# Performance work log

Hardware: AMD Instinct MI355X
Metric: run time of the kernel (lower is better)

The kernel has to match this reference:

```python
import jax, jax.numpy as jnp
import numpy as np

B, T, P, D, H = 32, 64, 196, 768, 12
HD = D // H   # MHA head dim = 64
F = D // H    # GAT per-head out features = 64


def _grid_adj(num_patches):
    g = int(np.sqrt(num_patches))
    a = np.zeros((num_patches, num_patches), np.int32)
    for i in range(num_patches):
        a[i, i] = 1
        r, c = divmod(i, g)
        for dr in (-1, 0, 1):
            for dc in (-1, 0, 1):
                if dr == 0 and dc == 0:
                    continue
                nr, nc = r + dr, c + dc
                if 0 <= nr < g and 0 <= nc < g:
                    a[i, nr * g + nc] = 1
    return a


def setup_inputs():
    key = jax.random.key(0)
    ks = jax.random.split(key, 32)
    s = 0.02
    ta = jax.random.randint(ks[2], (B, T, T), 0, 2).astype(jnp.int32)
    ta = jnp.maximum(jnp.maximum(ta, ta.transpose(0, 2, 1)), jnp.eye(T, dtype=jnp.int32))
    return {
        'text_features': jax.random.normal(ks[0], (B, T, D), jnp.float32),
        'image_features': jax.random.normal(ks[1], (B, P, D), jnp.float32),
        'clip_text': jax.random.normal(ks[3], (B, 512), jnp.float32),
        'clip_image': jax.random.normal(ks[4], (B, 512), jnp.float32),
        'logit_scale': jnp.float32(4.6052),  # ln(100), CLIP default
        'wq': jax.random.normal(ks[5], (D, D), jnp.float32) * s,
        'bq': jnp.zeros((D,), jnp.float32),
        'wk': jax.random.normal(ks[6], (D, D), jnp.float32) * s,
        'bk': jnp.zeros((D,), jnp.float32),
        'wv': jax.random.normal(ks[7], (D, D), jnp.float32) * s,
        'bv': jnp.zeros((D,), jnp.float32),
        'wo': jax.random.normal(ks[8], (D, D), jnp.float32) * s,
        'bo': jnp.zeros((D,), jnp.float32),
        'Wt': jax.random.normal(ks[9], (D, H * F), jnp.float32) * s,
        'at': jax.random.normal(ks[10], (2 * F, 1), jnp.float32) * s,
        'Wi': jax.random.normal(ks[11], (D, H * F), jnp.float32) * s,
        'ai': jax.random.normal(ks[12], (2 * F, 1), jnp.float32) * s,
        'Wp': jax.random.normal(ks[13], (512, D), jnp.float32) * s,
        'bp': jnp.zeros((D,), jnp.float32),
        'f1w': jax.random.normal(ks[14], (3, 16), jnp.float32) * 0.3,
        'f1b': jnp.zeros((16,), jnp.float32),
        'f2w': jax.random.normal(ks[15], (16, 3), jnp.float32) * 0.3,
        'f2b': jnp.zeros((3,), jnp.float32),
        'c1w': jax.random.normal(ks[16], (D, D // 2), jnp.float32) * s,
        'c1b': jnp.zeros((D // 2,), jnp.float32),
        'c2w': jax.random.normal(ks[17], (D // 2, 2), jnp.float32) * s,
        'c2b': jnp.zeros((2,), jnp.float32),
        'text_adj': ta,
        'image_adj': jnp.asarray(_grid_adj(P)),
    }


def _gat(h, adj, W, a):
    # h: [N, D], adj: [N, N] (0/1), W: [D, H*F], a: [2F, 1]
    N = h.shape[0]
    Wh = (h @ W).reshape(N, H, F)
    # e_ij = leakyrelu(a^T [Wh_i ; Wh_j]) decomposed to avoid the N*N*2F concat tensor
    src = jnp.einsum('nhf,f->nh', Wh, a[:F, 0])   # [N, H]
    dst = jnp.einsum('nhf,f->nh', Wh, a[F:, 0])   # [N, H]
    e = jax.nn.leaky_relu(src[:, None, :] + dst[None, :, :], 0.2)  # [N, N, H]
    e = jnp.where(adj[:, :, None] > 0, e, jnp.float32(-9e15))
    att = jax.nn.softmax(e, axis=1)               # softmax over neighbors j
    hp = jnp.einsum('ijh,jhf->ihf', att, Wh)       # [N, H, F]
    return jax.nn.elu(hp.reshape(N, H * F))


def reference(text_features, image_features, clip_text, clip_image, logit_scale,
              wq, bq, wk, bk, wv, bv, wo, bo, Wt, at, Wi, ai, Wp, bp,
              f1w, f1b, f2w, f2b, c1w, c1b, c2w, c2b, text_adj, image_adj):
    # token-level cross attention (text queries, image keys/values)
    q = (text_features @ wq + bq).reshape(B, T, H, HD)
    k = (image_features @ wk + bk).reshape(B, P, H, HD)
    v = (image_features @ wv + bv).reshape(B, P, H, HD)
    scores = jnp.einsum('bthd,bphd->bhtp', q, k) / jnp.sqrt(jnp.float32(HD))
    upd = jnp.einsum('bhtp,bphd->bthd', jax.nn.softmax(scores, axis=-1), v)
    upd = upd.reshape(B, T, D) @ wo + bo           # [B, T, D]
    c = jnp.einsum('btd,bpd->btp', upd, image_features)
    s_token = jnp.mean(jnp.diagonal(c, axis1=-2, axis2=-1), axis=1)  # [B]
    f_token = upd.mean(axis=1)                     # [B, D]
    # per-sample GATs, batched via vmap
    tg = jax.vmap(lambda h, a_: _gat(h, a_, Wt, at))(text_features, text_adj)
    ig = jax.vmap(lambda h: _gat(h, image_adj, Wi, ai))(image_features)
    tgf = tg.mean(axis=1)
    igf = ig.mean(axis=1)

    def cos(x, y):
        nx = jnp.maximum(jnp.linalg.norm(x, axis=-1), 1e-8)
        ny = jnp.maximum(jnp.linalg.norm(y, axis=-1), 1e-8)
        return jnp.sum(x * y, axis=-1) / (nx * ny)

    s_phrase = cos(tgf, igf)
    s_global = jnp.exp(logit_scale) * cos(clip_text, clip_image)
    f_global = clip_text @ Wp + bp
    scores3 = jax.lax.stop_gradient(jnp.stack([s_token, s_phrase, s_global], axis=1))
    w = jax.nn.sigmoid(jax.nn.gelu(scores3 @ f1w + f1b, approximate=False) @ f2w + f2b)
    f_agg = w[:, 0:1] * f_token + w[:, 1:2] * tgf + w[:, 2:3] * f_global
    logits = jax.nn.relu(f_agg @ c1w + c1b) @ c2w + c2b  # dropout inactive (eval)
    return logits
```

## Files before the change

kernel.cpp:

```cpp
#include <hip/hip_runtime.h>
#include <hip/hip_bf16.h>
#include <math.h>

#define B 32
#define T 64
#define P 196
#define D 768
#define H 12

typedef __attribute__((ext_vector_type(8))) short short8;
typedef __attribute__((ext_vector_type(4))) float floatx4;

__device__ __forceinline__ float wave_sum(float v) {
#pragma unroll
  for (int o = 32; o > 0; o >>= 1) v += __shfl_xor(v, o);
  return v;
}
__device__ __forceinline__ unsigned short f2bf(float x) {
  unsigned u = __float_as_uint(x);
  u += 0x7FFFu + ((u >> 16) & 1u);
  return (unsigned short)(u >> 16);
}
__device__ __forceinline__ float bf2f(unsigned short x) {
  return __uint_as_float((unsigned)x << 16);
}
__device__ __forceinline__ float fexp(float x) { return __expf(x); }
__device__ __forceinline__ float frcp(float x) { return __builtin_amdgcn_rcpf(x); }
__device__ __forceinline__ void async_cp16(const unsigned short* g, unsigned short* l) {
  __builtin_amdgcn_global_load_lds(
      (const __attribute__((address_space(1))) unsigned int*)g,
      (__attribute__((address_space(3))) unsigned int*)l, 16, 0, 0);
}
__device__ __forceinline__ int xcd_remap(int orig, int nwg) {
  const int q = nwg >> 3, r = nwg & 7;
  const int x = orig & 7, o = orig >> 3;
  return (x < r ? x * (q + 1) : r * (q + 1) + (x - r) * q) + o;
}

struct WPack {
  const float* src[6];
  unsigned short* dst[6];
};
__global__ __launch_bounds__(256) void prep_kernel(
    WPack p,
    const float* __restrict__ text, unsigned short* __restrict__ text_bf, int n40,
    const float* __restrict__ img, unsigned short* __restrict__ img_bf, int n41,
    const float* __restrict__ bq, const float* __restrict__ bk,
    const float* __restrict__ bv,
    float* __restrict__ bt, float* __restrict__ bi, float* __restrict__ stok) {
  const int bid = blockIdx.x;
  if (bid < 3456) {
    __shared__ float tile[32][33];
    const int z = bid / 576, rem = bid % 576;
    const int bx = rem % 24, by = rem / 24;
    const float* W = p.src[z];
    unsigned short* Wt = p.dst[z];
    const int tx = threadIdx.x & 31, ty = threadIdx.x >> 5;
    const int n0 = bx * 32, k0 = by * 32;
#pragma unroll
    for (int r = 0; r < 4; ++r)
      tile[ty + 8 * r][tx] = W[(size_t)(k0 + ty + 8 * r) * D + n0 + tx];
    __syncthreads();
#pragma unroll
    for (int r = 0; r < 4; ++r)
      Wt[(size_t)(n0 + ty + 8 * r) * D + k0 + tx] = f2bf(tile[tx][ty + 8 * r]);
  } else if (bid < 9696) {
    int i = (bid - 3456) * 256 + threadIdx.x;
    const float* X;
    unsigned short* Y;
    int idx;
    if (i < n40) { X = text; Y = text_bf; idx = i; }
    else if (i < n40 + n41) { X = img; Y = img_bf; idx = i - n40; }
    else return;
    float4 vv = ((const float4*)X)[idx];
    ushort4 o;
    o.x = f2bf(vv.x); o.y = f2bf(vv.y); o.z = f2bf(vv.z); o.w = f2bf(vv.w);
    ((ushort4*)Y)[idx] = o;
  } else {
    int i = (bid - 9696) * 256 + threadIdx.x;
    if (i < 32) stok[i] = 0.f;
    if (i < 768) { bt[i] = bq[i]; bi[i] = bk[i]; }
    else if (i < 1536) { bt[i] = 0.f; bi[i] = bv[i - 768]; }
    else if (i < 2304) { bi[i] = 0.f; }
  }
}

struct GemmJob {
  const unsigned short* A;
  const unsigned short* Bt;
  const float* bias;
  void* C;
  int N, K, lda, ldb, colTiles;
};

template <bool BF16OUT>
__device__ __forceinline__ void gemm_body(const GemmJob& j, int bx, int by, int tid) {
  __shared__ unsigned short As[3][128][32];
  __shared__ unsigned short Bs[3][128][32];
  const int lane = tid & 63;
  const int w = tid >> 6;
  const int quad = lane >> 4;
  const int l15 = lane & 15;
  const int row0 = by * 128;
  const int col0 = bx * 128;
  const int m_off = (w & 1) * 64;
  const int n_off = (w >> 1) * 64;
  const int N = j.N, K = j.K;

  const int srow = 16 * w + (lane >> 2);
  const int scol = (((lane & 3) ^ ((lane >> 3) & 3))) * 8;
  const unsigned short* gA0 = j.A + (size_t)(row0 + srow) * j.lda + scol;
  const unsigned short* gA1 = j.A + (size_t)(row0 + srow + 64) * j.lda + scol;
  const unsigned short* gB0 = j.Bt + (size_t)(col0 + srow) * j.ldb + scol;
  const unsigned short* gB1 = j.Bt + (size_t)(col0 + srow + 64) * j.ldb + scol;

  const int rdc = (quad ^ ((l15 >> 1) & 3)) * 8;

  floatx4 acc[4][4] = {};

#define STAGE(buf, kk)                                   \
  do {                                                   \
    async_cp16(gA0 + (kk), &As[buf][16 * w][0]);         \
    async_cp16(gA1 + (kk), &As[buf][64 + 16 * w][0]);    \
    async_cp16(gB0 + (kk), &Bs[buf][16 * w][0]);         \
    async_cp16(gB1 + (kk), &Bs[buf][64 + 16 * w][0]);    \
  } while (0)

  STAGE(0, 0);
  STAGE(1, 32);

  for (int k0 = 0; k0 < K; k0 += 96) {
#pragma unroll
    for (int sub = 0; sub < 3; ++sub) {
      const int kk = k0 + sub * 32;
      const int cur = sub;
      const int nxt = (sub + 2) % 3;
      if (kk + 64 < K) {
        STAGE(nxt, kk + 64);
        asm volatile("s_waitcnt vmcnt(8)" ::: "memory");
      } else if (kk + 32 < K) {
        asm volatile("s_waitcnt vmcnt(4)" ::: "memory");
      } else {
        asm volatile("s_waitcnt vmcnt(0)" ::: "memory");
      }
      __builtin_amdgcn_s_barrier();
      __builtin_amdgcn_sched_barrier(0);

      short8 af[4], bfr[4];
#pragma unroll
      for (int i = 0; i < 4; ++i)
        af[i] = *(const short8*)&As[cur][m_off + 16 * i + l15][rdc];
#pragma unroll
      for (int jj = 0; jj < 4; ++jj)
        bfr[jj] = *(const short8*)&Bs[cur][n_off + 16 * jj + l15][rdc];
#pragma unroll
      for (int i = 0; i < 4; ++i)
#pragma unroll
        for (int jj = 0; jj < 4; ++jj)
          acc[i][jj] = __builtin_amdgcn_mfma_f32_16x16x32_bf16(af[i], bfr[jj], acc[i][jj], 0, 0, 0);

      __builtin_amdgcn_sched_barrier(0);
      __builtin_amdgcn_s_barrier();
    }
  }
#undef STAGE

#pragma unroll
  for (int jj = 0; jj < 4; ++jj) {
    const int cg = col0 + n_off + 16 * jj + l15;
    const float bv = j.bias ? j.bias[cg] : 0.0f;
#pragma unroll
    for (int i = 0; i < 4; ++i) {
      const int rbase = row0 + m_off + 16 * i + quad * 4;
#pragma unroll
      for (int r = 0; r < 4; ++r) {
        const float val = acc[i][jj][r] + bv;
        const size_t idx = (size_t)(rbase + r) * N + cg;
        if (BF16OUT) ((unsigned short*)j.C)[idx] = f2bf(val);
        else ((float*)j.C)[idx] = val;
      }
    }
  }
}

__global__ __launch_bounds__(256) void gemm_mfma_dual_bf16(GemmJob j0, GemmJob j1,
                                                           int split, int total) {
  const bool first = ((int)blockIdx.x < split);
  const GemmJob& j = first ? j0 : j1;
  const int orig = first ? blockIdx.x : (blockIdx.x - split);
  const int bid = xcd_remap(orig, first ? split : total - split);
  const int bx = bid % j.colTiles;
  const int by = bid / j.colTiles;
  gemm_body<true>(j, bx, by, threadIdx.x);
}

__global__ __launch_bounds__(256) void gemm_mfma_dual_f32(GemmJob j0, GemmJob j1,
                                                          int split, int total) {
  const bool first = ((int)blockIdx.x < split);
  const GemmJob& j = first ? j0 : j1;
  const int orig = first ? blockIdx.x : (blockIdx.x - split);
  const int bid = xcd_remap(orig, first ? split : total - split);
  const int bx = bid % j.colTiles;
  const int by = bid / j.colTiles;
  gemm_body<false>(j, bx, by, threadIdx.x);
}


__device__ __forceinline__ void attn_body(
    char* smem, int h, int b,
    const unsigned short* __restrict__ qa, const unsigned short* __restrict__ kvw,
    unsigned short* __restrict__ attout) {
  const int tid = threadIdx.x, lane = tid & 63, w = tid >> 6;
  const int quad = lane >> 4, l15 = lane & 15;

  unsigned short (*Ks)[72] = (unsigned short(*)[72])smem;
  unsigned short (*Ps)[16][232] = (unsigned short(*)[16][232])smem;
  unsigned short (*VT)[232] = (unsigned short(*)[232])(smem + 29952);

  for (int i = tid; i < P * 8; i += 256) {
    const int p = i >> 3, dg = i & 7;
    const short8 k8 =
        *(const short8*)(kvw + (size_t)(b * P + p) * 2304 + h * 64 + dg * 8);
    *(short8*)&Ks[p][dg * 8] = k8;
  }
  {
    const int d = lane;
    const unsigned short* vbase = kvw + (size_t)b * P * 2304 + 768 + h * 64 + d;
    for (int pb = w; pb < 28; pb += 4) {
      short8 v;
#pragma unroll
      for (int z = 0; z < 8; ++z) {
        const int p = pb * 8 + z;
        v[z] = (p < P) ? (short)vbase[(size_t)p * 2304] : (short)0;
      }
      *(short8*)&VT[d][pb * 8] = v;
    }
  }
  __syncthreads();

  short8 aq[2];
#pragma unroll
  for (int ks = 0; ks < 2; ++ks)
    aq[ks] = *(const short8*)(qa + (size_t)(b * T + 16 * w + l15) * 1536 + h * 64 +
                              32 * ks + quad * 8);

  floatx4 sc[13];
#pragma unroll
  for (int tile = 0; tile < 13; ++tile) {
    int p = tile * 16 + l15;
    if (p > 195) p = 195;
    short8 bk0 = *(const short8*)&Ks[p][quad * 8];
    short8 bk1 = *(const short8*)&Ks[p][32 + quad * 8];
    floatx4 c = {};
    c = __builtin_amdgcn_mfma_f32_16x16x32_bf16(aq[0], bk0, c, 0, 0, 0);
    c = __builtin_amdgcn_mfma_f32_16x16x32_bf16(aq[1], bk1, c, 0, 0, 0);
    sc[tile] = c;
  }

  float mx[4] = {-3.4e38f, -3.4e38f, -3.4e38f, -3.4e38f};
#pragma unroll
  for (int tile = 0; tile < 13; ++tile)
#pragma unroll
    for (int r = 0; r < 4; ++r) {
      float s = sc[tile][r] * 0.125f;
      if (tile == 12 && l15 >= 4) s = -3.0e38f;
      sc[tile][r] = s;
      mx[r] = fmaxf(mx[r], s);
    }
#pragma unroll
  for (int off = 1; off < 16; off <<= 1)
#pragma unroll
    for (int r = 0; r < 4; ++r) mx[r] = fmaxf(mx[r], __shfl_xor(mx[r], off));

  float sm[4] = {};
#pragma unroll
  for (int tile = 0; tile < 13; ++tile)
#pragma unroll
    for (int r = 0; r < 4; ++r) {
      float e = fexp(sc[tile][r] - mx[r]);
      sc[tile][r] = e;
      sm[r] += e;
    }
#pragma unroll
  for (int off = 1; off < 16; off <<= 1)
#pragma unroll
    for (int r = 0; r < 4; ++r) sm[r] += __shfl_xor(sm[r], off);
  float inv[4];
#pragma unroll
  for (int r = 0; r < 4; ++r) inv[r] = frcp(sm[r]);

  __syncthreads();

#pragma unroll
  for (int tile = 0; tile < 13; ++tile)
#pragma unroll
    for (int r = 0; r < 4; ++r)
      Ps[w][quad * 4 + r][tile * 16 + l15] = f2bf(sc[tile][r]);
#pragma unroll
  for (int r = 0; r < 4; ++r)
    Ps[w][quad * 4 + r][208 + l15] = 0;

  floatx4 oc[4] = {};
#pragma unroll
  for (int ks = 0; ks < 7; ++ks) {
    short8 pa = *(const short8*)&Ps[w][l15][ks * 32 + quad * 8];
#pragma unroll
    for (int nt = 0; nt < 4; ++nt) {
      short8 bv = *(const short8*)&VT[nt * 16 + l15][ks * 32 + quad * 8];
      oc[nt] = __builtin_amdgcn_mfma_f32_16x16x32_bf16(pa, bv, oc[nt], 0, 0, 0);
    }
  }

#pragma unroll
  for (int nt = 0; nt < 4; ++nt)
#pragma unroll
    for (int r = 0; r < 4; ++r)
      attout[(size_t)(b * T + 16 * w + quad * 4 + r) * 768 + h * 64 + nt * 16 + l15] =
          f2bf(oc[nt][r] * inv[r]);
}

__device__ __forceinline__ void text_gat_body(
    char* smem, int h, int b,
    const unsigned short* __restrict__ Wh, int ldw, const int* __restrict__ adj,
    const float* __restrict__ at, float* __restrict__ tgf) {
  const int tid = threadIdx.x, lane = tid & 63, w = tid >> 6;
  const int quad = lane >> 4, l15 = lane & 15;

  unsigned short (*VT)[72] = (unsigned short(*)[72])smem;
  unsigned short (*Ps)[16][72] = (unsigned short(*)[16][72])(smem + 9216);
  float* srcs = (float*)(smem + 18432);
  float* dsts = (float*)(smem + 18688);
  float (*redc)[64] = (float(*)[64])(smem + 18944);
  float* asv = (float*)(smem + 19968);
  float* adv = (float*)(smem + 20224);

  if (tid < 64) { asv[tid] = at[tid]; adv[tid] = at[64 + tid]; }
  {
    const int f = lane;
    const unsigned short* wbase = Wh + (size_t)(b * T) * ldw + h * 64 + f;
    for (int nb = w; nb < 8; nb += 4) {
      short8 v;
#pragma unroll
      for (int z = 0; z < 8; ++z)
        v[z] = (short)wbase[(size_t)(nb * 8 + z) * ldw];
      *(short8*)&VT[f][nb * 8] = v;
    }
  }
  __syncthreads();

  if (tid < 64) {
    float s = 0.f, dd = 0.f;
#pragma unroll 8
    for (int f = 0; f < 64; ++f) {
      const float wv = bf2f(VT[f][tid]);
      s += wv * asv[f];
      dd += wv * adv[f];
    }
    srcs[tid] = s;
    dsts[tid] = dd;
  }
  __syncthreads();

  const int i = 16 * w + l15;
  const float si = srcs[i];
  const int* ar = adj + (size_t)b * T * T + i * 64;
  float sm = 0.f;
#pragma unroll 8
  for (int jj = 0; jj < 16; ++jj) {
    const int j = 4 * jj + quad;
    float e = si + dsts[j];
    e = (e >= 0.f) ? e : 0.2f * e;
    const float p = (ar[j] != 0) ? fexp(e) : 0.f;
    sm += p;
    Ps[w][l15][j] = f2bf(p);
  }
  sm += __shfl_xor(sm, 16);
  sm += __shfl_xor(sm, 32);
  const float inv = frcp(sm);

  floatx4 oc[4] = {};
#pragma unroll
  for (int ks = 0; ks < 2; ++ks) {
    const short8 pa = *(const short8*)&Ps[w][l15][ks * 32 + quad * 8];
#pragma unroll
    for (int nt = 0; nt < 4; ++nt) {
      const short8 bv = *(const short8*)&VT[nt * 16 + l15][ks * 32 + quad * 8];
      oc[nt] = __builtin_amdgcn_mfma_f32_16x16x32_bf16(pa, bv, oc[nt], 0, 0, 0);
    }
  }

  float accd[4] = {};
#pragma unroll
  for (int r = 0; r < 4; ++r) {
    const float invr = __shfl(inv, quad * 4 + r);
#pragma unroll
    for (int nt = 0; nt < 4; ++nt) {
      const float hp = oc[nt][r] * invr;
      accd[nt] += (hp > 0.f) ? hp : (fexp(hp) - 1.0f);
    }
  }
#pragma unroll
  for (int nt = 0; nt < 4; ++nt) {
    accd[nt] += __shfl_xor(accd[nt], 16);
    accd[nt] += __shfl_xor(accd[nt], 32);
  }
  if (quad == 0) {
#pragma unroll
    for (int nt = 0; nt < 4; ++nt) redc[w][nt * 16 + l15] = accd[nt];
  }
  __syncthreads();
  if (w == 0) {
    const float tot = redc[0][lane] + redc[1][lane] + redc[2][lane] + redc[3][lane];
    tgf[b * D + h * 64 + lane] = tot * (1.0f / T);
  }
}

__device__ __forceinline__ void image_gat_body(
    char* smem, int h, int b,
    const unsigned short* __restrict__ Wh, int ldw, const float* __restrict__ ai,
    const int* __restrict__ adj, float* __restrict__ igf) {
  const int tid = threadIdx.x, lane = tid & 63, w = tid >> 6;
  const int quad = lane >> 4, l15 = lane & 15;

  unsigned short (*VT)[232] = (unsigned short(*)[232])smem;
  unsigned short (*Ps)[232] = (unsigned short(*)[232])(smem + 29696);
  float* srcs = (float*)(smem + 37120);
  float* dsts = (float*)(smem + 37904);
  float* asv = (float*)(smem + 38688);
  float* adv = (float*)(smem + 38944);

  if (tid < 64) { asv[tid] = ai[tid]; adv[tid] = ai[64 + tid]; }
  {
    const int f = lane;
    const unsigned short* wbase = Wh + (size_t)(b * P) * ldw + h * 64 + f;
    for (int nb = w; nb < 28; nb += 4) {
      short8 v;
#pragma unroll
      for (int z = 0; z < 8; ++z) {
        const int p = nb * 8 + z;
        v[z] = (p < P) ? (short)wbase[(size_t)p * ldw] : (short)0;
      }
      *(short8*)&VT[f][nb * 8] = v;
    }
  }
  __syncthreads();

  if (tid < P) {
    float s = 0.f, dd = 0.f;
#pragma unroll 8
    for (int f = 0; f < 64; ++f) {
      const float wv = bf2f(VT[f][tid]);
      s += wv * asv[f];
      dd += wv * adv[f];
    }
    srcs[tid] = s;
    dsts[tid] = dd;
  }
  __syncthreads();

  const int rloc = tid >> 4;
  const int cslot = tid & 15;
  float accw = 0.f;

  for (int tile = 0; tile < 13; ++tile) {
    const int i = tile * 16 + rloc;
    const int ii = (i < P) ? i : (P - 1);
    const float si = srcs[ii];
    const int* ar = adj + ii * P;
    int msk[13];
#pragma unroll
    for (int k = 0; k < 13; ++k) {
      const int jc = k * 16 + cslot;
      msk[k] = (jc < P) ? ar[jc] : 0;
    }
    float pvv[13];
    float sm = 0.f;
#pragma unroll
    for (int k = 0; k < 13; ++k) {
      const int jc = k * 16 + cslot;
      float p = 0.f;
      if (jc < P && msk[k] != 0) {
        float e = si + dsts[jc];
        e = (e >= 0.f) ? e : 0.2f * e;
        p = fexp(e);
      }
      pvv[k] = p;
      sm += p;
    }
    sm += __shfl_xor(sm, 1);
    sm += __shfl_xor(sm, 2);
    sm += __shfl_xor(sm, 4);
    sm += __shfl_xor(sm, 8);
    const float inv = frcp(sm);
#pragma unroll
    for (int k = 0; k < 13; ++k)
      Ps[rloc][k * 16 + cslot] = f2bf(pvv[k] * inv);
    Ps[rloc][208 + cslot] = 0;
    __syncthreads();

    floatx4 oc = {};
#pragma unroll
    for (int ks = 0; ks < 7; ++ks) {
      const short8 pa = *(const short8*)&Ps[l15][ks * 32 + quad * 8];
      const short8 bvv = *(const short8*)&VT[w * 16 + l15][ks * 32 + quad * 8];
      oc = __builtin_amdgcn_mfma_f32_16x16x32_bf16(pa, bvv, oc, 0, 0, 0);
    }
#pragma unroll
    for (int r = 0; r < 4; ++r) {
      const int io = tile * 16 + quad * 4 + r;
      if (io < P) {
        const float hp = oc[r];
        accw += (hp > 0.f) ? hp : (fexp(hp) - 1.0f);
      }
    }
    __syncthreads();
  }

  accw += __shfl_xor(accw, 16);
  accw += __shfl_xor(accw, 32);
  if (quad == 0)
    igf[b * D + h * 64 + w * 16 + l15] = accw * (1.0f / P);
}

__device__ __forceinline__ void fglob_body(
    char* smem, int jt, int b,
    const float* __restrict__ clip_t, const float* __restrict__ Wp,
    const float* __restrict__ bp, float* __restrict__ fglob) {
  const int j = threadIdx.x & 63, kc = threadIdx.x >> 6;
  float s = 0.f;
  const float* ct = clip_t + b * 512;
#pragma unroll 4
  for (int k = kc * 128; k < kc * 128 + 128; ++k)
    s += ct[k] * Wp[(size_t)k * D + jt * 64 + j];
  float (*red)[64] = (float(*)[64])smem;
  red[kc][j] = s;
  __syncthreads();
  if (kc == 0)
    fglob[b * D + jt * 64 + j] = red[0][j] + red[1][j] + red[2][j] + red[3][j] + bp[jt * 64 + j];
}

__global__ __launch_bounds__(256) void mid_kernel(
    const unsigned short* __restrict__ qa_bf, const unsigned short* __restrict__ kvw_bf,
    unsigned short* __restrict__ att_bf,
    const int* __restrict__ text_adj, const float* __restrict__ at,
    float* __restrict__ tgf,
    const unsigned short* __restrict__ whi, int ldw_i,
    const float* __restrict__ ai, const int* __restrict__ image_adj,
    float* __restrict__ igf,
    const float* __restrict__ clip_t, const float* __restrict__ Wp,
    const float* __restrict__ bp, float* __restrict__ fglob) {
  __shared__ __align__(16) char smem[59648];
  const int h = blockIdx.x, b = blockIdx.y, op = blockIdx.z;
  if (op == 0)
    attn_body(smem, h, b, qa_bf, kvw_bf, att_bf);
  else if (op == 1)
    text_gat_body(smem, h, b, qa_bf + 768, 1536, text_adj, at, tgf);
  else if (op == 2)
    image_gat_body(smem, h, b, whi, ldw_i, ai, image_adj, igf);
  else
    fglob_body(smem, h, b, clip_t, Wp, bp, fglob);
}

__global__ __launch_bounds__(256) void token_kernel(
    const float* __restrict__ upd0, const float* __restrict__ upd1,
    const float* __restrict__ img,
    float* __restrict__ f_token, float* __restrict__ s_token) {
  const int jt = blockIdx.x, b = blockIdx.y;
  const int l = threadIdx.x & 63, tg = threadIdx.x >> 6;
  const int d = jt * 64 + l;
  float fs = 0.f, ss = 0.f;
#pragma unroll 4
  for (int tt = 0; tt < 16; ++tt) {
    const int t = tg * 16 + tt;
    const size_t idx = (size_t)(b * T + t) * D + d;
    const float u = upd0[idx] + upd1[idx];
    fs += u;
    ss += u * img[(size_t)(b * P + t) * D + d];
  }
  __shared__ float red[4][64];
  __shared__ float sred[4];
  red[tg][l] = fs;
  const float sw = wave_sum(ss);
  if (l == 0) sred[tg] = sw;
  __syncthreads();
  if (tg == 0) {
    f_token[(size_t)b * D + d] =
        (red[0][l] + red[1][l] + red[2][l] + red[3][l]) * (1.0f / T);
    if (threadIdx.x == 0)
      atomicAdd(&s_token[b], (sred[0] + sred[1] + sred[2] + sred[3]) * (1.0f / T));
  }
}

__global__ __launch_bounds__(256) void xc1_kernel(
    const float* __restrict__ ftok, const float* __restrict__ tgf,
    const float* __restrict__ fglob, const float* __restrict__ c1w,
    float* __restrict__ Xc) {
  const int jt = blockIdx.x;
  const int r = blockIdx.y;
  const int b = r & 31, which = r >> 5;
  const float* src = (which == 0 ? ftok : which == 1 ? tgf : fglob) + (size_t)b * D;
  const int j = threadIdx.x & 63, kc = threadIdx.x >> 6;
  const int col = jt * 64 + j;
  float s = 0.f;
#pragma unroll 4
  for (int k = kc * 192; k < kc * 192 + 192; ++k)
    s += src[k] * c1w[(size_t)k * 384 + col];
  __shared__ float red[4][64];
  red[kc][j] = s;
  __syncthreads();
  if (kc == 0)
    Xc[(size_t)r * 384 + col] = red[0][j] + red[1][j] + red[2][j] + red[3][j];
}

__device__ __forceinline__ float block_sum(float v, float* red4) {
  v = wave_sum(v);
  __syncthreads();
  if ((threadIdx.x & 63) == 0) red4[threadIdx.x >> 6] = v;
  __syncthreads();
  return red4[0] + red4[1] + red4[2] + red4[3];
}

__global__ __launch_bounds__(256) void final_kernel(
    const float* __restrict__ tgf, const float* __restrict__ igf,
    const float* __restrict__ clip_t, const float* __restrict__ clip_i,
    const float* __restrict__ logit_scale, const float* __restrict__ s_token,
    const float* __restrict__ Xc,
    const float* __restrict__ f1w, const float* __restrict__ f1b,
    const float* __restrict__ f2w, const float* __restrict__ f2b,
    const float* __restrict__ c1b,
    const float* __restrict__ c2w, const float* __restrict__ c2b,
    float* __restrict__ out) {
  const int b = blockIdx.x, tid = threadIdx.x;
  __shared__ float red[4];
  __shared__ float sres[4];
  __shared__ float hid[384];

  float d0 = 0.f, d1 = 0.f, d2 = 0.f;
  for (int i = tid; i < D; i += 256) {
    float x = tgf[b * D + i], y = igf[b * D + i];
    d0 += x * y; d1 += x * x; d2 += y * y;
  }
  float dot_ti = block_sum(d0, red);
  float n_t = sqrtf(block_sum(d1, red));
  float n_i = sqrtf(block_sum(d2, red));
  float s_phrase = dot_ti / (fmaxf(n_t, 1e-8f) * fmaxf(n_i, 1e-8f));

  float c0 = 0.f, c1 = 0.f, c2 = 0.f;
  for (int i = tid; i < 512; i += 256) {
    float x = clip_t[b * 512 + i], y = clip_i[b * 512 + i];
    c0 += x * y; c1 += x * x; c2 += y * y;
  }
  float dc = block_sum(c0, red);
  float nt2 = sqrtf(block_sum(c1, red));
  float ni2 = sqrtf(block_sum(c2, red));
  float s_global = expf(logit_scale[0]) * dc / (fmaxf(nt2, 1e-8f) * fmaxf(ni2, 1e-8f));

  if (tid == 0) {
    float s3[3] = { s_token[b], s_phrase, s_global };
    float h1[16];
    for (int j = 0; j < 16; ++j) {
      float a = f1b[j];
      for (int i2 = 0; i2 < 3; ++i2) a += s3[i2] * f1w[i2 * 16 + j];
      h1[j] = 0.5f * a * (1.0f + erff(a * 0.70710678118654752f));
    }
    for (int j = 0; j < 3; ++j) {
      float a = f2b[j];
      for (int i2 = 0; i2 < 16; ++i2) a += h1[i2] * f2w[i2 * 3 + j];
      sres[j] = 1.0f / (1.0f + expf(-a));
    }
  }
  __syncthreads();
  const float w0 = sres[0], w1 = sres[1], w2 = sres[2];

  for (int j = tid; j < 384; j += 256) {
    const float a = w0 * Xc[(size_t)b * 384 + j] +
                    w1 * Xc[(size_t)(32 + b) * 384 + j] +
                    w2 * Xc[(size_t)(64 + b) * 384 + j] + c1b[j];
    hid[j] = fmaxf(a, 0.0f);
  }
  __syncthreads();

  float p0 = 0.f, p1 = 0.f;
  for (int k2 = tid; k2 < 384; k2 += 256) {
    p0 += hid[k2] * c2w[k2 * 2 + 0];
    p1 += hid[k2] * c2w[k2 * 2 + 1];
  }
  p0 = block_sum(p0, red);
  p1 = block_sum(p1, red);
  if (tid == 0) {
    out[b * 2 + 0] = p0 + c2b[0];
    out[b * 2 + 1] = p1 + c2b[1];
  }
}

extern "C" void kernel_launch(void* const* d_in, const int* in_sizes, int n_in,
                              void* d_out, int out_size, void* d_ws, size_t ws_size,
                              hipStream_t stream) {
  const float* text   = (const float*)d_in[0];
  const float* img    = (const float*)d_in[1];
  const float* clip_t = (const float*)d_in[2];
  const float* clip_i = (const float*)d_in[3];
  const float* lscale = (const float*)d_in[4];
  const float* wq = (const float*)d_in[5];
  const float* bq = (const float*)d_in[6];
  const float* wk = (const float*)d_in[7];
  const float* bk = (const float*)d_in[8];
  const float* wv = (const float*)d_in[9];
  const float* bv = (const float*)d_in[10];
  const float* wo = (const float*)d_in[11];
  const float* bo = (const float*)d_in[12];
  const float* Wt = (const float*)d_in[13];
  const float* at = (const float*)d_in[14];
  const float* Wi = (const float*)d_in[15];
  const float* ai = (const float*)d_in[16];
  const float* Wp = (const float*)d_in[17];
  const float* bp = (const float*)d_in[18];
  const float* f1w = (const float*)d_in[19];
  const float* f1b = (const float*)d_in[20];
  const float* f2w = (const float*)d_in[21];
  const float* f2b = (const float*)d_in[22];
  const float* c1w = (const float*)d_in[23];
  const float* c1b = (const float*)d_in[24];
  const float* c2w = (const float*)d_in[25];
  const float* c2b = (const float*)d_in[26];
  const int* text_adj  = (const int*)d_in[27];
  const int* image_adj = (const int*)d_in[28];
  float* out = (float*)d_out;

  const size_t nTD = (size_t)B * T * D;
  const size_t nPD = (size_t)B * P * D;
  const size_t nWW = (size_t)D * D;

  float* fbuf = (float*)d_ws;
  size_t o = 0;
  float* upd0    = fbuf + o; o += nTD;
  float* upd1    = fbuf + o; o += nTD;
  float* ftok    = fbuf + o; o += (size_t)B * D;
  float* stok    = fbuf + o; o += 32;
  float* tgf     = fbuf + o; o += (size_t)B * D;
  float* igf     = fbuf + o; o += (size_t)B * D;
  float* fglob   = fbuf + o; o += (size_t)B * D;
  float* bcat_t  = fbuf + o; o += 1536;
  float* bcat_i3 = fbuf + o; o += 2304;
  float* Xc      = fbuf + o; o += (size_t)96 * 384;
  unsigned short* sbuf = (unsigned short*)(fbuf + o);
  size_t so = 0;
  unsigned short* kvw_bf    = sbuf + so; so += 3 * nPD;
  unsigned short* qa_bf     = sbuf + so; so += 2 * nTD;
  unsigned short* text_bf   = sbuf + so; so += nTD;
  unsigned short* img_bf    = sbuf + so; so += nPD;
  unsigned short* att_bf    = sbuf + so; so += nTD;
  unsigned short* wcat_txt  = sbuf + so; so += 2 * nWW;
  unsigned short* wcat_img3 = sbuf + so; so += 3 * nWW;
  unsigned short* wo_t      = sbuf + so; so += nWW;

  WPack wp;
  wp.src[0] = wq; wp.dst[0] = wcat_txt;
  wp.src[1] = Wt; wp.dst[1] = wcat_txt + nWW;
  wp.src[2] = wk; wp.dst[2] = wcat_img3;
  wp.src[3] = wv; wp.dst[3] = wcat_img3 + nWW;
  wp.src[4] = Wi; wp.dst[4] = wcat_img3 + 2 * nWW;
  wp.src[5] = wo; wp.dst[5] = wo_t;
  {
    const int n40 = (int)(nTD / 4), n41 = (int)(nPD / 4);
    prep_kernel<<<9708, 256, 0, stream>>>(wp, text, text_bf, n40, img, img_bf, n41,
                                          bq, bk, bv, bcat_t, bcat_i3, stok);
  }

  const int MT = B * T;
  const int MP = B * P;

  GemmJob jimg;
  jimg.A = img_bf; jimg.Bt = wcat_img3; jimg.bias = bcat_i3; jimg.C = kvw_bf;
  jimg.N = 2304; jimg.K = D; jimg.lda = D; jimg.ldb = D; jimg.colTiles = 2304 / 128;
  GemmJob jtxt;
  jtxt.A = text_bf; jtxt.Bt = wcat_txt; jtxt.bias = bcat_t; jtxt.C = qa_bf;
  jtxt.N = 1536; jtxt.K = D; jtxt.lda = D; jtxt.ldb = D; jtxt.colTiles = 1536 / 128;
  const int splitBlocks = (2304 / 128) * (MP / 128);
  const int totalBlocks = splitBlocks + (1536 / 128) * (MT / 128);
  gemm_mfma_dual_bf16<<<totalBlocks, 256, 0, stream>>>(jimg, jtxt, splitBlocks, totalBlocks);

  const unsigned short* whi_bf = kvw_bf + 1536;
  mid_kernel<<<dim3(H, B, 4), 256, 0, stream>>>(
      qa_bf, kvw_bf, att_bf,
      text_adj, at, tgf,
      whi_bf, 2304, ai, image_adj, igf,
      clip_t, Wp, bp, fglob);

  GemmJob jwo0;
  jwo0.A = att_bf; jwo0.Bt = wo_t; jwo0.bias = bo; jwo0.C = upd0;
  jwo0.N = D; jwo0.K = 384; jwo0.lda = D; jwo0.ldb = D; jwo0.colTiles = D / 128;
  GemmJob jwo1;
  jwo1.A = att_bf + 384; jwo1.Bt = wo_t + 384; jwo1.bias = nullptr; jwo1.C = upd1;
  jwo1.N = D; jwo1.K = 384; jwo1.lda = D; jwo1.ldb = D; jwo1.colTiles = D / 128;
  const int woHalf = (D / 128) * (MT / 128);
  gemm_mfma_dual_f32<<<2 * woHalf, 256, 0, stream>>>(jwo0, jwo1, woHalf, 2 * woHalf);

  token_kernel<<<dim3(12, B), 256, 0, stream>>>(upd0, upd1, img, ftok, stok);
  xc1_kernel<<<dim3(6, 96), 256, 0, stream>>>(ftok, tgf, fglob, c1w, Xc);
  final_kernel<<<B, 256, 0, stream>>>(tgf, igf, clip_t, clip_i, lscale, stok, Xc,
                                      f1w, f1b, f2w, f2b, c1b, c2w, c2b, out);
}
```

Measured before the change: 263.7 us.

## Software-pipeline GEMM LDS fragment loads with register double buffering

Restructures the bf16 MFMA GEMM main loop so that the LDS fragments for the next k-step are read into a second register set while the MFMAs for the current step run. This uses one barrier per k-step instead of two and tightens the vmcnt waits. The goal is to hide LDS read latency and barrier stalls behind matrix-core work. The cost is more registers, and the loop is now unrolled by six steps. When K is not a multiple of 192, the extra phases still issue MFMAs on stale fragments.

```diff
diff --git a/kernel.cpp b/kernel.cpp
--- a/kernel.cpp
+++ b/kernel.cpp
@@ -117,6 +117,8 @@
   const int rdc = (quad ^ ((l15 >> 1) & 3)) * 8;
 
   floatx4 acc[4][4] = {};
+  short8 fA[4], fB_[4];
+  short8 gA_[4], gB_[4];
 
 #define STAGE(buf, kk)                                   \
   do {                                                   \
@@ -126,42 +128,53 @@
     async_cp16(gB1 + (kk), &Bs[buf][64 + 16 * w][0]);    \
   } while (0)
 
+  auto RD = [&](short8 (&AF)[4], short8 (&BF)[4], int buf) {
+#pragma unroll
+    for (int i = 0; i < 4; ++i)
+      AF[i] = *(const short8*)&As[buf][m_off + 16 * i + l15][rdc];
+#pragma unroll
+    for (int j2 = 0; j2 < 4; ++j2)
+      BF[j2] = *(const short8*)&Bs[buf][n_off + 16 * j2 + l15][rdc];
+  };
+  auto MM = [&](short8 (&AF)[4], short8 (&BF)[4]) {
+#pragma unroll
+    for (int i = 0; i < 4; ++i)
+#pragma unroll
+      for (int j2 = 0; j2 < 4; ++j2)
+        acc[i][j2] = __builtin_amdgcn_mfma_f32_16x16x32_bf16(AF[i], BF[j2], acc[i][j2], 0, 0, 0);
+  };
+  auto PHASE = [&](short8 (&curA)[4], short8 (&curB)[4],
+                   short8 (&nxtA)[4], short8 (&nxtB)[4],
+                   int stageBuf, int readBuf, int kk) {
+    if (kk + 64 < K) {
+      STAGE(stageBuf, kk + 64);
+      asm volatile("s_waitcnt vmcnt(4) lgkmcnt(0)" ::: "memory");
+      __builtin_amdgcn_s_barrier();
+      __builtin_amdgcn_sched_barrier(0);
+      RD(nxtA, nxtB, readBuf);
+    } else if (kk + 32 < K) {
+      asm volatile("s_waitcnt vmcnt(0) lgkmcnt(0)" ::: "memory");
+      __builtin_amdgcn_s_barrier();
+      __builtin_amdgcn_sched_barrier(0);
+      RD(nxtA, nxtB, readBuf);
+    }
+    MM(curA, curB);
+  };
+
   STAGE(0, 0);
   STAGE(1, 32);
-
-  for (int k0 = 0; k0 < K; k0 += 96) {
-#pragma unroll
-    for (int sub = 0; sub < 3; ++sub) {
-      const int kk = k0 + sub * 32;
-      const int cur = sub;
-      const int nxt = (sub + 2) % 3;
-      if (kk + 64 < K) {
-        STAGE(nxt, kk + 64);
-        asm volatile("s_waitcnt vmcnt(8)" ::: "memory");
-      } else if (kk + 32 < K) {
-        asm volatile("s_waitcnt vmcnt(4)" ::: "memory");
-      } else {
-        asm volatile("s_waitcnt vmcnt(0)" ::: "memory");
-      }
-      __builtin_amdgcn_s_barrier();
-      __builtin_amdgcn_sched_barrier(0);
-
-      short8 af[4], bfr[4];
-#pragma unroll
-      for (int i = 0; i < 4; ++i)
-        af[i] = *(const short8*)&As[cur][m_off + 16 * i + l15][rdc];
-#pragma unroll
-      for (int jj = 0; jj < 4; ++jj)
-        bfr[jj] = *(const short8*)&Bs[cur][n_off + 16 * jj + l15][rdc];
-#pragma unroll
-      for (int i = 0; i < 4; ++i)
-#pragma unroll
-        for (int jj = 0; jj < 4; ++jj)
-          acc[i][jj] = __builtin_amdgcn_mfma_f32_16x16x32_bf16(af[i], bfr[jj], acc[i][jj], 0, 0, 0);
-
-      __builtin_amdgcn_sched_barrier(0);
-      __builtin_amdgcn_s_barrier();
-    }
+  asm volatile("s_waitcnt vmcnt(4)" ::: "memory");
+  __builtin_amdgcn_s_barrier();
+  __builtin_amdgcn_sched_barrier(0);
+  RD(fA, fB_, 0);
+
+  for (int k0 = 0; k0 < K; k0 += 192) {
+    PHASE(fA, fB_, gA_, gB_, 2, 1, k0);
+    PHASE(gA_, gB_, fA, fB_, 0, 2, k0 + 32);
+    PHASE(fA, fB_, gA_, gB_, 1, 0, k0 + 64);
+    PHASE(gA_, gB_, fA, fB_, 2, 1, k0 + 96);
+    PHASE(fA, fB_, gA_, gB_, 0, 2, k0 + 128);
+    PHASE(gA_, gB_, fA, fB_, 1, 0, k0 + 160);
   }
 #undef STAGE
 
```

After: 260.9 us. Within noise of the previous version (-1.0%).
